# Optimization experiments

Measured on AMD Instinct MI355X. Metric: run time of the kernel, lower is better.

The kernel has to match this reference:

```python
import jax, jax.numpy as jnp
import numpy as np

D = 1024
FFN = 1024
EPS_LN = 1e-5
EPS_GN = 1e-5

def _ln(x, w, b):
    m = x.mean(-1, keepdims=True)
    v = x.var(-1, keepdims=True)
    return (x - m) / jnp.sqrt(v + EPS_LN) * w + b

def setup_inputs() -> dict:
    key = jax.random.key(0)
    ks = jax.random.split(key, 24)
    p = lambda i, shp, s=0.02: jax.random.normal(ks[i], shp, jnp.float32) * s
    inp = {
        'x': jax.random.normal(ks[0], (8, 2048, D), jnp.float32),
        'state': jnp.zeros((8, D), jnp.float32),
        'ln1_w': jnp.ones((D,)), 'ln1_b': jnp.zeros((D,)),
        'ln2_w': jnp.ones((D,)), 'ln2_b': jnp.zeros((D,)),
        'gn_w': jnp.ones((D,)), 'gn_b': jnp.zeros((D,)),
        'grn_gamma': jnp.zeros((1, 1, D)), 'grn_beta': jnp.zeros((1, 1, D)),
        'decay': jnp.full((D,), -3.0, jnp.float32),
        'Wr': p(1, (D, D), 0.05), 'Wk': p(2, (D, D)), 'Wv': p(3, (D, D)),
        'Wg': p(4, (D, D), 0.05), 'Wa': p(5, (D, D)), 'Wb': p(6, (D, D)),
        'Wout': p(7, (D, D)), 'Wffnout': p(8, (D, D)),
        'Wfk': p(9, (D, FFN)), 'bfk': jnp.zeros((FFN,)),
        'Wfv': p(10, (FFN, D)), 'bfv': jnp.zeros((D,)),
        'Wfr': p(11, (D, D)), 'bfr': jnp.zeros((D,)),
    }
    return inp

def reference(x, state, ln1_w, ln1_b, ln2_w, ln2_b, gn_w, gn_b, grn_gamma, grn_beta, decay, Wr, Wk, Wv, Wg, Wa, Wb, Wout, Wffnout, Wfk, bfk, Wfv, bfv, Wfr, bfr):
    B, T, Dd = x.shape
    xx = _ln(x, ln1_w, ln1_b)
    shifted = jnp.pad(xx, ((0, 0), (1, 0), (0, 0)))[:, :-1]  # ZeroPad2d((0,0,1,-1))
    xm = 0.5 * (xx + shifted)
    r = xm @ Wr
    k = xm @ Wk
    v = xm @ Wv
    a = xm @ Wa
    b = xm @ Wb
    g = jax.nn.sigmoid(xm @ Wg)
    w = jnp.exp(-jnp.exp(decay))  # [D]
    u = k * v + a * b  # [B,T,D]
    def step(s, ut):
        s = s * w + ut
        return s, s
    final_state, states = jax.lax.scan(step, state, jnp.swapaxes(u, 0, 1))
    states = jnp.swapaxes(states, 0, 1)  # [B,T,D]
    # GroupNorm(dim//32, dim) applied over flattened (B*T, D)
    G = Dd // 32
    s4 = states.reshape(B, T, G, 32)
    m = s4.mean(-1, keepdims=True)
    va = s4.var(-1, keepdims=True)
    norm_states = ((s4 - m) / jnp.sqrt(va + EPS_GN)).reshape(B, T, Dd) * gn_w + gn_b
    mixed_out = (jax.nn.sigmoid(r) * norm_states * g) @ Wout
    x = x + mixed_out  # dropout is identity at inference
    xx2 = _ln(x, ln2_w, ln2_b)
    k_ffn = jnp.square(jax.nn.relu(xx2 @ Wfk + bfk))
    h = k_ffn @ Wfv + bfv  # [B,T,D]
    # GRN: L2 norm over time dim (dim=1), mean over channels
    gx = jnp.sqrt(jnp.sum(h * h, axis=1, keepdims=True))  # [B,1,D]
    nx = gx / (gx.mean(-1, keepdims=True) + 1e-6)
    ffn_hidden = grn_gamma * (h * nx) + grn_beta + h
    ffn_out = (jax.nn.sigmoid(xx2 @ Wfr + bfr) * ffn_hidden) @ Wffnout
    x = x + ffn_out
    return (x, final_state)
```

## Files before the change

kernel.cpp:

```cpp
#include <hip/hip_runtime.h>
#include <hip/hip_bf16.h>
#include <math.h>

#define D_DIM 1024
#define T_DIM 2048
#define B_DIM 8
#define M_DIM (B_DIM * T_DIM)
#define SZ ((size_t)M_DIM * D_DIM)
#define NW 11
#define CCH 16
#define LCH 128

typedef __bf16 bf16_t;
typedef __bf16 bf16x8 __attribute__((ext_vector_type(8)));
typedef __bf16 bf16x4 __attribute__((ext_vector_type(4)));
typedef float f32x4 __attribute__((ext_vector_type(4)));

typedef const __attribute__((address_space(1))) void* as1_const_ptr;
typedef __attribute__((address_space(3))) void* as3_ptr;

__device__ __forceinline__ void load_lds_16(const void* g, void* l) {
    __builtin_amdgcn_global_load_lds((as1_const_ptr)g, (as3_ptr)l, 16, 0, 0);
}

__device__ __forceinline__ float sigmoid_f(float x) { return 1.f / (1.f + expf(-x)); }

template<int NT, int MODE>
__global__ void __launch_bounds__(512, 4)
gemm2_kernel(const bf16_t* __restrict__ A, const bf16_t* __restrict__ Bt,
             void* __restrict__ out0, void* __restrict__ out1,
             const float* __restrict__ bias0, const float* __restrict__ bias1,
             const void* __restrict__ other)
{
    constexpr int K = D_DIM;
    __shared__ bf16_t sA[2][256 * 32];
    __shared__ bf16_t sB[2][128 * 32];
    __shared__ float gsum[8][64];
    const int tid  = threadIdx.x;
    const int wave = tid >> 6, lane = tid & 63;

    const int lin = blockIdx.x;
    const int xcd = lin & 7;
    const int idx = lin >> 3;
    const int mt  = xcd * 8 + idx / NT;
    const int nt  = idx % NT;
    const int m0 = mt * 256, n0 = nt * 128;

    const int wm = (wave & 3) * 64;
    const int wn = (wave >> 2) * 64;

    const int rl = lane >> 2;
    const int cc = lane & 3;
    const int scol = (cc ^ ((rl >> 1) & 3)) * 8;
    const bf16_t* gA = A  + (size_t)(m0 + wave * 32 + rl) * K + scol;
    const bf16_t* gB = Bt + (size_t)(n0 + wave * 16 + rl) * K + scol;
    const int lofsA = (wave * 32) * 32;
    const int lofsB = (wave * 16) * 32;

    f32x4 acc[4][4] = {};

    const int fr = lane & 15;
    const int quad = lane >> 4;
    const int qs = (quad ^ ((fr >> 1) & 3)) * 8;

    load_lds_16(gA,                   &sA[0][lofsA]);
    load_lds_16(gA + (size_t)16 * K,  &sA[0][lofsA + 16 * 32]);
    load_lds_16(gB,                   &sB[0][lofsB]);
    __syncthreads();

    int cur = 0;
    for (int kk = 0; kk < K; kk += 32) {
        if (kk + 32 < K) {
            const int nb = cur ^ 1;
            load_lds_16(gA + kk + 32,                   &sA[nb][lofsA]);
            load_lds_16(gA + (size_t)16 * K + kk + 32,  &sA[nb][lofsA + 16 * 32]);
            load_lds_16(gB + kk + 32,                   &sB[nb][lofsB]);
        }
        bf16x8 af[4], bq[4];
        #pragma unroll
        for (int i = 0; i < 4; i++)
            af[i] = *(const bf16x8*)(&sA[cur][(wm + i * 16 + fr) * 32 + qs]);
        #pragma unroll
        for (int j = 0; j < 4; j++)
            bq[j] = *(const bf16x8*)(&sB[cur][(wn + j * 16 + fr) * 32 + qs]);
        #pragma unroll
        for (int i = 0; i < 4; i++)
            #pragma unroll
            for (int j = 0; j < 4; j++)
                acc[i][j] = __builtin_amdgcn_mfma_f32_16x16x32_bf16(af[i], bq[j], acc[i][j], 0, 0, 0);
        __syncthreads();
        cur ^= 1;
    }

    float hs[4] = {0.f, 0.f, 0.f, 0.f};

    #pragma unroll
    for (int i = 0; i < 4; i++) {
        #pragma unroll
        for (int j = 0; j < 4; j++) {
            const int col = n0 + wn + j * 16 + fr;
            #pragma unroll
            for (int r = 0; r < 4; r++) {
                const int row = m0 + wm + i * 16 + quad * 4 + r;
                float v = acc[i][j][r];
                if constexpr (MODE == 3) {
                    const size_t id = (size_t)row * D_DIM + col;
                    ((float*)out0)[id] = v + ((const float*)other)[id];
                } else if constexpr (MODE == 5) {
                    const int w = nt >> 3;
                    const int lc = col & (D_DIM - 1);
                    const size_t id = (size_t)row * D_DIM + lc;
                    if (w == 0) {
                        float v2 = fmaxf(v + bias0[lc], 0.f);
                        ((bf16_t*)out0)[id] = (bf16_t)(v2 * v2);
                    } else {
                        ((bf16_t*)out1)[id] = (bf16_t)sigmoid_f(v + bias1[lc]);
                    }
                } else if constexpr (MODE == 6) {
                    const int w = nt >> 3;
                    const size_t id = (size_t)row * D_DIM + (col & (D_DIM - 1));
                    if (w == 0) ((bf16_t*)out0)[id] = (bf16_t)sigmoid_f(v);
                    else        ((bf16_t*)out1)[id] = (bf16_t)sigmoid_f(v);
                } else {
                    const float h = v + bias0[col];
                    ((float*)out0)[(size_t)row * D_DIM + col] = h;
                    hs[j] += h * h;
                }
            }
        }
    }

    if constexpr (MODE == 7) {
        #pragma unroll
        for (int j = 0; j < 4; j++) {
            float t = hs[j];
            t += __shfl_xor(t, 16);
            t += __shfl_xor(t, 32);
            if (lane < 16) gsum[wave][j * 16 + fr] = t;
        }
        __syncthreads();
        if (tid < 128) {
            const int p = tid >> 6, jf = tid & 63;
            const float tot = gsum[4 * p + 0][jf] + gsum[4 * p + 1][jf]
                            + gsum[4 * p + 2][jf] + gsum[4 * p + 3][jf];
            ((float*)out1)[(size_t)mt * D_DIM + n0 + p * 64 + jf] = tot;
        }
    }
}

__global__ void __launch_bounds__(256, 2)
gemm_uv_kernel(const bf16_t* __restrict__ A, const bf16_t* __restrict__ Wt4,
               float* __restrict__ u)
{
    constexpr int K = D_DIM;
    constexpr size_t WSZ_E = (size_t)D_DIM * D_DIM;
    __shared__ bf16_t sA[2][128 * 32];
    __shared__ bf16_t sB1[2][128 * 32];
    __shared__ bf16_t sB2[2][128 * 32];
    const int tid  = threadIdx.x;
    const int wave = tid >> 6, lane = tid & 63;

    const int lin = blockIdx.x;
    const int xcd = lin & 7;
    const int idx = lin >> 3;
    const int mt  = xcd * 16 + (idx >> 3);
    const int nt  = idx & 7;
    const int m0 = mt * 128, n0 = nt * 128;

    const int wm = (wave & 1) * 64, wn = (wave >> 1) * 64;

    const int rl = lane >> 2;
    const int cc = lane & 3;
    const int scol = (cc ^ ((rl >> 1) & 3)) * 8;
    const int srow = wave * 32 + rl;
    const bf16_t* gA  = A   + (size_t)(m0 + srow) * K + scol;
    const bf16_t* gB0 = Wt4 + (size_t)(n0 + srow) * K + scol;
    const int lofs = (wave * 32) * 32;

    const int fr = lane & 15;
    const int quad = lane >> 4;
    const int qs = (quad ^ ((fr >> 1) & 3)) * 8;

    auto kloop2 = [&](const bf16_t* gB1, const bf16_t* gB2,
                      f32x4 (&acc1)[4][4], f32x4 (&acc2)[4][4]) {
        load_lds_16(gA,                    &sA[0][lofs]);
        load_lds_16(gA  + (size_t)16 * K,  &sA[0][lofs + 16 * 32]);
        load_lds_16(gB1,                   &sB1[0][lofs]);
        load_lds_16(gB1 + (size_t)16 * K,  &sB1[0][lofs + 16 * 32]);
        load_lds_16(gB2,                   &sB2[0][lofs]);
        load_lds_16(gB2 + (size_t)16 * K,  &sB2[0][lofs + 16 * 32]);
        __syncthreads();
        int cur = 0;
        for (int kk = 0; kk < K; kk += 32) {
            if (kk + 32 < K) {
                const int nb = cur ^ 1;
                load_lds_16(gA  + kk + 32,                   &sA[nb][lofs]);
                load_lds_16(gA  + (size_t)16 * K + kk + 32,  &sA[nb][lofs + 16 * 32]);
                load_lds_16(gB1 + kk + 32,                   &sB1[nb][lofs]);
                load_lds_16(gB1 + (size_t)16 * K + kk + 32,  &sB1[nb][lofs + 16 * 32]);
                load_lds_16(gB2 + kk + 32,                   &sB2[nb][lofs]);
                load_lds_16(gB2 + (size_t)16 * K + kk + 32,  &sB2[nb][lofs + 16 * 32]);
            }
            bf16x8 af[4], b1[4], b2[4];
            #pragma unroll
            for (int i = 0; i < 4; i++)
                af[i] = *(const bf16x8*)(&sA[cur][(wm + i * 16 + fr) * 32 + qs]);
            #pragma unroll
            for (int j = 0; j < 4; j++) {
                b1[j] = *(const bf16x8*)(&sB1[cur][(wn + j * 16 + fr) * 32 + qs]);
                b2[j] = *(const bf16x8*)(&sB2[cur][(wn + j * 16 + fr) * 32 + qs]);
            }
            #pragma unroll
            for (int i = 0; i < 4; i++)
                #pragma unroll
                for (int j = 0; j < 4; j++) {
                    acc1[i][j] = __builtin_amdgcn_mfma_f32_16x16x32_bf16(af[i], b1[j], acc1[i][j], 0, 0, 0);
                    acc2[i][j] = __builtin_amdgcn_mfma_f32_16x16x32_bf16(af[i], b2[j], acc2[i][j], 0, 0, 0);
                }
            __syncthreads();
            cur ^= 1;
        }
    };

    f32x4 aKV[4][4] = {};
    f32x4 aT[4][4]  = {};
    f32x4 aB2[4][4] = {};

    kloop2(gB0, gB0 + WSZ_E, aKV, aT);
    #pragma unroll
    for (int i = 0; i < 4; i++)
        #pragma unroll
        for (int j = 0; j < 4; j++) {
            aKV[i][j] = aKV[i][j] * aT[i][j];
            aT[i][j] = f32x4{0.f, 0.f, 0.f, 0.f};
        }
    kloop2(gB0 + 2 * WSZ_E, gB0 + 3 * WSZ_E, aT, aB2);

    #pragma unroll
    for (int i = 0; i < 4; i++) {
        #pragma unroll
        for (int j = 0; j < 4; j++) {
            const int col = n0 + wn + j * 16 + fr;
            #pragma unroll
            for (int r = 0; r < 4; r++) {
                const int row = m0 + wm + i * 16 + quad * 4 + r;
                u[(size_t)row * D_DIM + col] =
                    aKV[i][j][r] + aT[i][j][r] * aB2[i][j][r];
            }
        }
    }
}

struct WList { const float* w[NW]; };

__global__ void __launch_bounds__(256)
transpose_cvt_kernel(WList wl, bf16_t* wt_base)
{
    __shared__ float tile[32][33];
    const float* W = wl.w[blockIdx.z];
    bf16_t* Wt = wt_base + (size_t)blockIdx.z * D_DIM * D_DIM;
    const int bx = blockIdx.x * 32, by = blockIdx.y * 32;
    const int tx = threadIdx.x, ty = threadIdx.y;
    #pragma unroll
    for (int i = 0; i < 32; i += 8)
        tile[ty + i][tx] = W[(size_t)(by + ty + i) * D_DIM + bx + tx];
    __syncthreads();
    #pragma unroll
    for (int i = 0; i < 32; i += 8)
        Wt[(size_t)(bx + ty + i) * D_DIM + by + tx] = (bf16_t)tile[tx][ty + i];
}

__global__ void __launch_bounds__(256)
ew_kernel(const float* __restrict__ decay, float* __restrict__ ew)
{
    const int d = blockIdx.x * 256 + threadIdx.x;
    if (d < D_DIM) ew[d] = expf(decay[d]);
}

__global__ void __launch_bounds__(256)
ln_shift_kernel(const float* __restrict__ x, const float* __restrict__ w,
                const float* __restrict__ bias, bf16_t* __restrict__ xm)
{
    const int row = blockIdx.x;
    const int t = row & (T_DIM - 1);
    const int d0 = threadIdx.x * 4;
    const float* xc = x + (size_t)row * D_DIM;
    f32x4 c = *(const f32x4*)(xc + d0);
    f32x4 p = {0.f, 0.f, 0.f, 0.f};
    if (t > 0) p = *(const f32x4*)(xc - D_DIM + d0);

    float sc = 0.f, qc = 0.f, sp = 0.f, qp = 0.f;
    #pragma unroll
    for (int e = 0; e < 4; e++) {
        sc += c[e]; qc += c[e] * c[e];
        sp += p[e]; qp += p[e] * p[e];
    }
    #pragma unroll
    for (int off = 32; off > 0; off >>= 1) {
        sc += __shfl_down(sc, off); qc += __shfl_down(qc, off);
        sp += __shfl_down(sp, off); qp += __shfl_down(qp, off);
    }
    __shared__ float red[16];
    const int wv = threadIdx.x >> 6, ln = threadIdx.x & 63;
    if (ln == 0) { red[wv] = sc; red[4 + wv] = qc; red[8 + wv] = sp; red[12 + wv] = qp; }
    __syncthreads();
    sc = red[0] + red[1] + red[2] + red[3];
    qc = red[4] + red[5] + red[6] + red[7];
    sp = red[8] + red[9] + red[10] + red[11];
    qp = red[12] + red[13] + red[14] + red[15];

    const float inv = 1.f / (float)D_DIM;
    const float mc = sc * inv, vc = qc * inv - mc * mc, rc = rsqrtf(vc + 1e-5f);
    const float mp = sp * inv, vp = qp * inv - mp * mp, rp = rsqrtf(vp + 1e-5f);

    bf16x4 o;
    #pragma unroll
    for (int e = 0; e < 4; e++) {
        const int d = d0 + e;
        const float wd = w[d], bd = bias[d];
        const float nc = (c[e] - mc) * rc * wd + bd;
        const float np = (t > 0) ? ((p[e] - mp) * rp * wd + bd) : 0.f;
        o[e] = (bf16_t)(0.5f * (nc + np));
    }
    *(bf16x4*)(xm + (size_t)row * D_DIM + d0) = o;
}

__global__ void __launch_bounds__(256)
scan1_kernel(float* __restrict__ u, const float* __restrict__ ew,
             float* __restrict__ carry)
{
    const int gid = blockIdx.x * 256 + threadIdx.x;
    const int d = gid & (D_DIM - 1);
    const int b = (gid >> 10) & (B_DIM - 1);
    const int c = gid >> 13;
    const float w = expf(-ew[d]);
    float s = 0.f;
    const size_t base = ((size_t)b * T_DIM + (size_t)c * LCH) * D_DIM + d;
    #pragma unroll 4
    for (int tl = 0; tl < LCH; tl++) {
        const size_t idx = base + (size_t)tl * D_DIM;
        s = fmaf(s, w, u[idx]);
        u[idx] = s;
    }
    carry[(size_t)(b * CCH + c) * D_DIM + d] = s;
}

__global__ void __launch_bounds__(256)
scan2_kernel(const float* __restrict__ s0, const float* __restrict__ ew,
             const float* __restrict__ carry, float* __restrict__ inc,
             float* __restrict__ fstate)
{
    const int gid = blockIdx.x * 256 + threadIdx.x;
    const int d = gid & (D_DIM - 1);
    const int b = gid >> 10;
    const float wL = expf(-(float)LCH * ew[d]);
    float s = s0[gid];
    #pragma unroll
    for (int c = 0; c < CCH; c++) {
        const size_t idx = (size_t)(b * CCH + c) * D_DIM + d;
        inc[idx] = s;
        s = fmaf(s, wL, carry[idx]);
    }
    fstate[gid] = s;
}

__global__ void __launch_bounds__(256)
mixed_kernel(const float* __restrict__ st, const float* __restrict__ inc,
             const float* __restrict__ ew, const bf16_t* __restrict__ sr,
             const bf16_t* __restrict__ g, const float* __restrict__ gnw,
             const float* __restrict__ gnb, bf16_t* __restrict__ outp)
{
    const int row = blockIdx.x;
    const int b = row >> 11;
    const int t = row & (T_DIM - 1);
    const int c = t >> 7, tl = t & (LCH - 1);
    const int d0 = threadIdx.x * 4;
    const size_t base = (size_t)row * D_DIM + d0;

    f32x4 lv = *(const f32x4*)(st + base);
    f32x4 iv = *(const f32x4*)(inc + (size_t)(b * CCH + c) * D_DIM + d0);
    f32x4 ev = *(const f32x4*)(ew + d0);

    float s[4];
    float sum = 0.f, sq = 0.f;
    #pragma unroll
    for (int e = 0; e < 4; e++) {
        s[e] = lv[e] + expf(-(float)(tl + 1) * ev[e]) * iv[e];
        sum += s[e]; sq += s[e] * s[e];
    }
    #pragma unroll
    for (int m = 1; m <= 4; m <<= 1) { sum += __shfl_xor(sum, m); sq += __shfl_xor(sq, m); }
    const float mean = sum * (1.f / 32.f);
    const float var  = sq * (1.f / 32.f) - mean * mean;
    const float rstd = rsqrtf(var + 1e-5f);

    bf16x4 rv = *(const bf16x4*)(sr + base);
    bf16x4 gv = *(const bf16x4*)(g + base);
    f32x4 wv = *(const f32x4*)(gnw + d0);
    f32x4 bv = *(const f32x4*)(gnb + d0);
    bf16x4 o;
    #pragma unroll
    for (int e = 0; e < 4; e++) {
        const float ns = (s[e] - mean) * rstd * wv[e] + bv[e];
        o[e] = (bf16_t)((float)rv[e] * ns * (float)gv[e]);
    }
    *(bf16x4*)(outp + base) = o;
}

__global__ void __launch_bounds__(256)
ln2_kernel(const float* __restrict__ x2, const float* __restrict__ w,
           const float* __restrict__ bias, bf16_t* __restrict__ xx2)
{
    const int row = blockIdx.x;
    const int d0 = threadIdx.x * 4;
    const float* xc = x2 + (size_t)row * D_DIM;
    f32x4 c = *(const f32x4*)(xc + d0);
    float sc = 0.f, qc = 0.f;
    #pragma unroll
    for (int e = 0; e < 4; e++) { sc += c[e]; qc += c[e] * c[e]; }
    #pragma unroll
    for (int off = 32; off > 0; off >>= 1) {
        sc += __shfl_down(sc, off); qc += __shfl_down(qc, off);
    }
    __shared__ float red[8];
    const int wv = threadIdx.x >> 6, ln = threadIdx.x & 63;
    if (ln == 0) { red[wv] = sc; red[4 + wv] = qc; }
    __syncthreads();
    sc = red[0] + red[1] + red[2] + red[3];
    qc = red[4] + red[5] + red[6] + red[7];
    const float inv = 1.f / (float)D_DIM;
    const float m = sc * inv, v = qc * inv - m * m, rs = rsqrtf(v + 1e-5f);
    bf16x4 o;
    #pragma unroll
    for (int e = 0; e < 4; e++) {
        const int d = d0 + e;
        o[e] = (bf16_t)((c[e] - m) * rs * w[d] + bias[d]);
    }
    *(bf16x4*)(xx2 + (size_t)row * D_DIM + d0) = o;
}

__global__ void __launch_bounds__(1024)
grn2_kernel(const float* __restrict__ partial, float* __restrict__ nx)
{
    const int b = blockIdx.x, d = threadIdx.x;
    float s = 0.f;
    #pragma unroll
    for (int c = 0; c < 8; c++) s += partial[(size_t)(b * 8 + c) * D_DIM + d];
    const float gx = sqrtf(s);
    float v = gx;
    #pragma unroll
    for (int off = 32; off > 0; off >>= 1) v += __shfl_down(v, off);
    __shared__ float red[16];
    if ((threadIdx.x & 63) == 0) red[threadIdx.x >> 6] = v;
    __syncthreads();
    float tot = 0.f;
    #pragma unroll
    for (int i = 0; i < 16; i++) tot += red[i];
    nx[b * D_DIM + d] = gx / (tot * (1.f / (float)D_DIM) + 1e-6f);
}

__global__ void __launch_bounds__(256)
frh_kernel(const float* __restrict__ h, const bf16_t* __restrict__ fr,
           const float* __restrict__ nx, const float* __restrict__ gamma,
           const float* __restrict__ beta, bf16_t* __restrict__ outp)
{
    const size_t gid = (size_t)blockIdx.x * 256 + threadIdx.x;
    const size_t i4 = gid * 4;
    const int d = (int)(i4 & (D_DIM - 1));
    const int b = (int)(i4 >> 21);
    f32x4 hv = *(const f32x4*)(h + i4);
    bf16x4 fv = *(const bf16x4*)(fr + i4);
    f32x4 nv = *(const f32x4*)(nx + (size_t)b * D_DIM + d);
    f32x4 gm = *(const f32x4*)(gamma + d);
    f32x4 bt = *(const f32x4*)(beta + d);
    bf16x4 o;
    #pragma unroll
    for (int e = 0; e < 4; e++) {
        const float hh = hv[e];
        const float val = gm[e] * (hh * nv[e]) + bt[e] + hh;
        o[e] = (bf16_t)((float)fv[e] * val);
    }
    *(bf16x4*)(outp + i4) = o;
}

extern "C" void kernel_launch(void* const* d_in, const int* in_sizes, int n_in,
                              void* d_out, int out_size, void* d_ws, size_t ws_size,
                              hipStream_t stream)
{
    (void)in_sizes; (void)n_in; (void)out_size; (void)ws_size;

    const float* x      = (const float*)d_in[0];
    const float* state0 = (const float*)d_in[1];
    const float* ln1_w  = (const float*)d_in[2];
    const float* ln1_b  = (const float*)d_in[3];
    const float* ln2_w  = (const float*)d_in[4];
    const float* ln2_b  = (const float*)d_in[5];
    const float* gn_w   = (const float*)d_in[6];
    const float* gn_b   = (const float*)d_in[7];
    const float* grn_g  = (const float*)d_in[8];
    const float* grn_b  = (const float*)d_in[9];
    const float* decay  = (const float*)d_in[10];
    const float* bfk    = (const float*)d_in[20];
    const float* bfv    = (const float*)d_in[22];
    const float* bfr    = (const float*)d_in[24];

    const size_t WSZ = (size_t)D_DIM * D_DIM;
    float*  F1 = (float*)d_ws;
    bf16_t* B0 = (bf16_t*)(F1 + SZ);
    bf16_t* B1 = B0 + SZ;
    bf16_t* B2 = B1 + SZ;
    bf16_t* B3 = B2 + SZ;
    bf16_t* WT = B3 + SZ;
    float*  carry   = (float*)(WT + NW * WSZ);
    float*  inc     = carry + (size_t)B_DIM * CCH * D_DIM;
    float*  partial = inc + (size_t)B_DIM * CCH * D_DIM;
    float*  nxp     = partial + (size_t)64 * D_DIM;
    float*  ewp     = nxp + (size_t)B_DIM * D_DIM;

    WList wl;
    const int widx[NW] = {11, 14, 12, 13, 15, 16, 17, 19, 23, 21, 18};
    for (int i = 0; i < NW; i++) wl.w[i] = (const float*)d_in[widx[i]];

    float* out_x  = (float*)d_out;
    float* out_st = out_x + SZ;

    transpose_cvt_kernel<<<dim3(32, 32, NW), dim3(32, 8), 0, stream>>>(wl, WT);
    ew_kernel<<<4, 256, 0, stream>>>(decay, ewp);
    ln_shift_kernel<<<M_DIM, 256, 0, stream>>>(x, ln1_w, ln1_b, B0);

    gemm2_kernel<16, 6><<<1024, 512, 0, stream>>>(
        B0, WT + 0 * WSZ, B2, B3, nullptr, nullptr, nullptr);
    gemm_uv_kernel<<<1024, 256, 0, stream>>>(B0, WT + 2 * WSZ, F1);

    scan1_kernel<<<(CCH * B_DIM * D_DIM) / 256, 256, 0, stream>>>(F1, ewp, carry);
    scan2_kernel<<<(B_DIM * D_DIM) / 256, 256, 0, stream>>>(state0, ewp, carry, inc, out_st);
    mixed_kernel<<<M_DIM, 256, 0, stream>>>(F1, inc, ewp, B2, B3, gn_w, gn_b, B1);

    gemm2_kernel<8, 3><<<512, 512, 0, stream>>>(
        B1, WT + 6 * WSZ, out_x, nullptr, nullptr, nullptr, x);
    ln2_kernel<<<M_DIM, 256, 0, stream>>>(out_x, ln2_w, ln2_b, B0);

    gemm2_kernel<16, 5><<<1024, 512, 0, stream>>>(
        B0, WT + 7 * WSZ, B1, B2, bfk, bfr, nullptr);
    gemm2_kernel<8, 7><<<512, 512, 0, stream>>>(
        B1, WT + 9 * WSZ, F1, partial, bfv, nullptr, nullptr);

    grn2_kernel<<<B_DIM, 1024, 0, stream>>>(partial, nxp);
    frh_kernel<<<M_DIM, 256, 0, stream>>>(F1, B2, nxp, grn_g, grn_b, B3);

    gemm2_kernel<8, 3><<<512, 512, 0, stream>>>(
        B3, WT + 10 * WSZ, out_x, nullptr, nullptr, nullptr, out_x);
}
```

Baseline: 855.3 us.

## Pair weight GEMMs sharing one A tile and enlarge M tile to 256

Replaces the concatenated-weight gemm2 launches (r/g and ffn-key/ffn-receptance) with a dual-B kernel in which each block loads one 256-row A tile and computes two 128-column outputs against two weight matrices, writing both epilogues. The uv kernel is retiled the same way, going to 512 threads with a 256-row M tile. The goal is to halve A-tile reloads and improve MFMA-to-load ratio. In exchange there are more accumulator registers per thread (two 4x4 f32x4 sets) and more LDS per block, which can limit occupancy under the stated 512x4 launch bounds.

```diff
diff --git a/kernel.cpp b/kernel.cpp
--- a/kernel.cpp
+++ b/kernel.cpp
@@ -106,21 +106,6 @@
                 if constexpr (MODE == 3) {
                     const size_t id = (size_t)row * D_DIM + col;
                     ((float*)out0)[id] = v + ((const float*)other)[id];
-                } else if constexpr (MODE == 5) {
-                    const int w = nt >> 3;
-                    const int lc = col & (D_DIM - 1);
-                    const size_t id = (size_t)row * D_DIM + lc;
-                    if (w == 0) {
-                        float v2 = fmaxf(v + bias0[lc], 0.f);
-                        ((bf16_t*)out0)[id] = (bf16_t)(v2 * v2);
-                    } else {
-                        ((bf16_t*)out1)[id] = (bf16_t)sigmoid_f(v + bias1[lc]);
-                    }
-                } else if constexpr (MODE == 6) {
-                    const int w = nt >> 3;
-                    const size_t id = (size_t)row * D_DIM + (col & (D_DIM - 1));
-                    if (w == 0) ((bf16_t*)out0)[id] = (bf16_t)sigmoid_f(v);
-                    else        ((bf16_t*)out1)[id] = (bf16_t)sigmoid_f(v);
                 } else {
                     const float h = v + bias0[col];
                     ((float*)out0)[(size_t)row * D_DIM + col] = h;
@@ -148,13 +133,15 @@
     }
 }
 
-__global__ void __launch_bounds__(256, 2)
-gemm_uv_kernel(const bf16_t* __restrict__ A, const bf16_t* __restrict__ Wt4,
-               float* __restrict__ u)
+template<int MODE>
+__global__ void __launch_bounds__(512, 4)
+gemm_pair_kernel(const bf16_t* __restrict__ A, const bf16_t* __restrict__ B1t,
+                 const bf16_t* __restrict__ B2t,
+                 void* __restrict__ out0, void* __restrict__ out1,
+                 const float* __restrict__ bias0, const float* __restrict__ bias1)
 {
     constexpr int K = D_DIM;
-    constexpr size_t WSZ_E = (size_t)D_DIM * D_DIM;
-    __shared__ bf16_t sA[2][128 * 32];
+    __shared__ bf16_t sA[2][256 * 32];
     __shared__ bf16_t sB1[2][128 * 32];
     __shared__ bf16_t sB2[2][128 * 32];
     const int tid  = threadIdx.x;
@@ -163,43 +150,136 @@
     const int lin = blockIdx.x;
     const int xcd = lin & 7;
     const int idx = lin >> 3;
-    const int mt  = xcd * 16 + (idx >> 3);
+    const int mt  = xcd * 8 + (idx >> 3);
     const int nt  = idx & 7;
-    const int m0 = mt * 128, n0 = nt * 128;
-
-    const int wm = (wave & 1) * 64, wn = (wave >> 1) * 64;
+    const int m0 = mt * 256, n0 = nt * 128;
+
+    const int wm = (wave & 3) * 64;
+    const int wn = (wave >> 2) * 64;
 
     const int rl = lane >> 2;
     const int cc = lane & 3;
     const int scol = (cc ^ ((rl >> 1) & 3)) * 8;
-    const int srow = wave * 32 + rl;
-    const bf16_t* gA  = A   + (size_t)(m0 + srow) * K + scol;
-    const bf16_t* gB0 = Wt4 + (size_t)(n0 + srow) * K + scol;
-    const int lofs = (wave * 32) * 32;
+    const bf16_t* gA  = A   + (size_t)(m0 + wave * 32 + rl) * K + scol;
+    const bf16_t* gB1 = B1t + (size_t)(n0 + wave * 16 + rl) * K + scol;
+    const bf16_t* gB2 = B2t + (size_t)(n0 + wave * 16 + rl) * K + scol;
+    const int lofsA = (wave * 32) * 32;
+    const int lofsB = (wave * 16) * 32;
+
+    f32x4 acc1[4][4] = {}, acc2[4][4] = {};
 
     const int fr = lane & 15;
     const int quad = lane >> 4;
     const int qs = (quad ^ ((fr >> 1) & 3)) * 8;
 
+    load_lds_16(gA,                   &sA[0][lofsA]);
+    load_lds_16(gA + (size_t)16 * K,  &sA[0][lofsA + 16 * 32]);
+    load_lds_16(gB1,                  &sB1[0][lofsB]);
+    load_lds_16(gB2,                  &sB2[0][lofsB]);
+    __syncthreads();
+
+    int cur = 0;
+    for (int kk = 0; kk < K; kk += 32) {
+        if (kk + 32 < K) {
+            const int nb = cur ^ 1;
+            load_lds_16(gA + kk + 32,                   &sA[nb][lofsA]);
+            load_lds_16(gA + (size_t)16 * K + kk + 32,  &sA[nb][lofsA + 16 * 32]);
+            load_lds_16(gB1 + kk + 32,                  &sB1[nb][lofsB]);
+            load_lds_16(gB2 + kk + 32,                  &sB2[nb][lofsB]);
+        }
+        bf16x8 af[4], b1[4], b2[4];
+        #pragma unroll
+        for (int i = 0; i < 4; i++)
+            af[i] = *(const bf16x8*)(&sA[cur][(wm + i * 16 + fr) * 32 + qs]);
+        #pragma unroll
+        for (int j = 0; j < 4; j++) {
+            b1[j] = *(const bf16x8*)(&sB1[cur][(wn + j * 16 + fr) * 32 + qs]);
+            b2[j] = *(const bf16x8*)(&sB2[cur][(wn + j * 16 + fr) * 32 + qs]);
+        }
+        #pragma unroll
+        for (int i = 0; i < 4; i++)
+            #pragma unroll
+            for (int j = 0; j < 4; j++) {
+                acc1[i][j] = __builtin_amdgcn_mfma_f32_16x16x32_bf16(af[i], b1[j], acc1[i][j], 0, 0, 0);
+                acc2[i][j] = __builtin_amdgcn_mfma_f32_16x16x32_bf16(af[i], b2[j], acc2[i][j], 0, 0, 0);
+            }
+        __syncthreads();
+        cur ^= 1;
+    }
+
+    #pragma unroll
+    for (int i = 0; i < 4; i++) {
+        #pragma unroll
+        for (int j = 0; j < 4; j++) {
+            const int col = n0 + wn + j * 16 + fr;
+            #pragma unroll
+            for (int r = 0; r < 4; r++) {
+                const int row = m0 + wm + i * 16 + quad * 4 + r;
+                const size_t id = (size_t)row * D_DIM + col;
+                const float v1 = acc1[i][j][r];
+                const float v2 = acc2[i][j][r];
+                if constexpr (MODE == 0) {
+                    ((bf16_t*)out0)[id] = (bf16_t)sigmoid_f(v1);
+                    ((bf16_t*)out1)[id] = (bf16_t)sigmoid_f(v2);
+                } else {
+                    float t = fmaxf(v1 + bias0[col], 0.f);
+                    ((bf16_t*)out0)[id] = (bf16_t)(t * t);
+                    ((bf16_t*)out1)[id] = (bf16_t)sigmoid_f(v2 + bias1[col]);
+                }
+            }
+        }
+    }
+}
+
+__global__ void __launch_bounds__(512, 4)
+gemm_uv_kernel(const bf16_t* __restrict__ A, const bf16_t* __restrict__ Wt4,
+               float* __restrict__ u)
+{
+    constexpr int K = D_DIM;
+    constexpr size_t WSZ_E = (size_t)D_DIM * D_DIM;
+    __shared__ bf16_t sA[2][256 * 32];
+    __shared__ bf16_t sB1[2][128 * 32];
+    __shared__ bf16_t sB2[2][128 * 32];
+    const int tid  = threadIdx.x;
+    const int wave = tid >> 6, lane = tid & 63;
+
+    const int lin = blockIdx.x;
+    const int xcd = lin & 7;
+    const int idx = lin >> 3;
+    const int mt  = xcd * 8 + (idx >> 3);
+    const int nt  = idx & 7;
+    const int m0 = mt * 256, n0 = nt * 128;
+
+    const int wm = (wave & 3) * 64;
+    const int wn = (wave >> 2) * 64;
+
+    const int rl = lane >> 2;
+    const int cc = lane & 3;
+    const int scol = (cc ^ ((rl >> 1) & 3)) * 8;
+    const bf16_t* gA  = A   + (size_t)(m0 + wave * 32 + rl) * K + scol;
+    const bf16_t* gB0 = Wt4 + (size_t)(n0 + wave * 16 + rl) * K + scol;
+    const int lofsA = (wave * 32) * 32;
+    const int lofsB = (wave * 16) * 32;
+
+    const int fr = lane & 15;
+    const int quad = lane >> 4;
+    const int qs = (quad ^ ((fr >> 1) & 3)) * 8;
+
     auto kloop2 = [&](const bf16_t* gB1, const bf16_t* gB2,
                       f32x4 (&acc1)[4][4], f32x4 (&acc2)[4][4]) {
-        load_lds_16(gA,                    &sA[0][lofs]);
-        load_lds_16(gA  + (size_t)16 * K,  &sA[0][lofs + 16 * 32]);
-        load_lds_16(gB1,                   &sB1[0][lofs]);
-        load_lds_16(gB1 + (size_t)16 * K,  &sB1[0][lofs + 16 * 32]);
-        load_lds_16(gB2,                   &sB2[0][lofs]);
-        load_lds_16(gB2 + (size_t)16 * K,  &sB2[0][lofs + 16 * 32]);
+        load_lds_16(gA,                   &sA[0][lofsA]);
+        load_lds_16(gA + (size_t)16 * K,  &sA[0][lofsA + 16 * 32]);
+        load_lds_16(gB1,                  &sB1[0][lofsB]);
+        load_lds_16(gB2,                  &sB2[0][lofsB]);
         __syncthreads();
         int cur = 0;
         for (int kk = 0; kk < K; kk += 32) {
             if (kk + 32 < K) {
                 const int nb = cur ^ 1;
-                load_lds_16(gA  + kk + 32,                   &sA[nb][lofs]);
-                load_lds_16(gA  + (size_t)16 * K + kk + 32,  &sA[nb][lofs + 16 * 32]);
-                load_lds_16(gB1 + kk + 32,                   &sB1[nb][lofs]);
-                load_lds_16(gB1 + (size_t)16 * K + kk + 32,  &sB1[nb][lofs + 16 * 32]);
-                load_lds_16(gB2 + kk + 32,                   &sB2[nb][lofs]);
-                load_lds_16(gB2 + (size_t)16 * K + kk + 32,  &sB2[nb][lofs + 16 * 32]);
+                load_lds_16(gA + kk + 32,                   &sA[nb][lofsA]);
+                load_lds_16(gA + (size_t)16 * K + kk + 32,  &sA[nb][lofsA + 16 * 32]);
+                load_lds_16(gB1 + kk + 32,                  &sB1[nb][lofsB]);
+                load_lds_16(gB2 + kk + 32,                  &sB2[nb][lofsB]);
             }
             bf16x8 af[4], b1[4], b2[4];
             #pragma unroll
@@ -528,9 +608,9 @@
     ew_kernel<<<4, 256, 0, stream>>>(decay, ewp);
     ln_shift_kernel<<<M_DIM, 256, 0, stream>>>(x, ln1_w, ln1_b, B0);
 
-    gemm2_kernel<16, 6><<<1024, 512, 0, stream>>>(
-        B0, WT + 0 * WSZ, B2, B3, nullptr, nullptr, nullptr);
-    gemm_uv_kernel<<<1024, 256, 0, stream>>>(B0, WT + 2 * WSZ, F1);
+    gemm_pair_kernel<0><<<512, 512, 0, stream>>>(
+        B0, WT + 0 * WSZ, WT + 1 * WSZ, B2, B3, nullptr, nullptr);
+    gemm_uv_kernel<<<512, 512, 0, stream>>>(B0, WT + 2 * WSZ, F1);
 
     scan1_kernel<<<(CCH * B_DIM * D_DIM) / 256, 256, 0, stream>>>(F1, ewp, carry);
     scan2_kernel<<<(B_DIM * D_DIM) / 256, 256, 0, stream>>>(state0, ewp, carry, inc, out_st);
@@ -540,8 +620,8 @@
         B1, WT + 6 * WSZ, out_x, nullptr, nullptr, nullptr, x);
     ln2_kernel<<<M_DIM, 256, 0, stream>>>(out_x, ln2_w, ln2_b, B0);
 
-    gemm2_kernel<16, 5><<<1024, 512, 0, stream>>>(
-        B0, WT + 7 * WSZ, B1, B2, bfk, bfr, nullptr);
+    gemm_pair_kernel<1><<<512, 512, 0, stream>>>(
+        B0, WT + 7 * WSZ, WT + 8 * WSZ, B1, B2, bfk, bfr);
     gemm2_kernel<8, 7><<<512, 512, 0, stream>>>(
         B1, WT + 9 * WSZ, F1, partial, bfv, nullptr, nullptr);
 
```

Measured after the change: 2.861 ms. 235% more time.
